# Kernel optimization log

Hardware: AMD Instinct MI355X
Metric: run time of the kernel (lower is better)

Reference implementation:

```python
import jax, jax.numpy as jnp
from jax import lax
import numpy as np

H = 512
W = 512
SIGMA = 0.1
IN_CH = [3, 66, 64, 64, 32, 32, 32, 16, 16]
OUT_CH = [64, 64, 64, 32, 32, 32, 16, 16, 16]
N_LAYERS = 9


def setup_inputs() -> dict:
    key = jax.random.key(0)
    ks = jax.random.split(key, 32)
    inp = {}
    inp['x'] = jax.random.uniform(ks[0], (3, 3, 1, 1), jnp.float32)  # query + 2 neighbor coords
    inp['neighbors'] = jax.random.uniform(ks[1], (2, 3, H, W), jnp.float32)
    inp['albedo_index'] = 4
    for i in range(N_LAYERS):
        kh = 1 if i == 0 else 3
        fan_in = IN_CH[i] * kh * kh
        inp[f'w{i}'] = jax.random.normal(ks[2 + i], (OUT_CH[i], IN_CH[i], kh, kh), jnp.float32) / np.sqrt(fan_in).astype(np.float32)
        inp[f'b{i}'] = jnp.zeros((OUT_CH[i],), jnp.float32)
    inp['wf'] = jax.random.normal(ks[20], (6, 16, 3, 3), jnp.float32) / np.sqrt(16 * 9).astype(np.float32)
    inp['bf'] = jnp.zeros((6,), jnp.float32)
    inp['albedos'] = 0.5 + jax.random.uniform(ks[21], (9, 3, H, W), jnp.float32)
    return inp


def _conv(x, w, b):
    y = lax.conv_general_dilated(x, w, (1, 1), 'VALID', dimension_numbers=('NCHW', 'OIHW', 'NCHW'))
    return y + b[None, :, None, None]


def _decoder(x, ws, bs, wf, bf):
    # coordconv constant [[ [0,2],[0,2] ], [ [0,0],[2,2] ]] with shape [2,2,2]
    coordconv = jnp.array([[[0., 2.], [0., 2.]], [[0., 0.], [2., 2.]]], dtype=x.dtype)
    for i in range(N_LAYERS):
        x = jnp.repeat(jnp.repeat(x, 2, axis=2), 2, axis=3)  # nearest upsample x2
        if i > 0:
            x = jnp.pad(x, ((0, 0), (0, 0), (1, 1), (1, 1)), mode='reflect')
        x = jax.nn.leaky_relu(_conv(x, ws[i], bs[i]), 0.01)
        if i == 0:
            cc = jnp.broadcast_to(coordconv[None], (x.shape[0],) + coordconv.shape)
            x = jnp.concatenate([x, cc], axis=1)  # -> 66 channels at 2x2
    x = jnp.pad(x, ((0, 0), (0, 0), (1, 1), (1, 1)), mode='reflect')
    return jnp.tanh(_conv(x, wf, bf))  # [B, 6, H, W]


def _grid_sample_border(img, grid):
    # bilinear, padding_mode='border', align_corners=False (matches torch grid_sample)
    N, C, Hh, Ww = img.shape
    gx = jnp.clip((grid[..., 0] + 1.0) * Ww / 2.0 - 0.5, 0.0, Ww - 1.0)
    gy = jnp.clip((grid[..., 1] + 1.0) * Hh / 2.0 - 0.5, 0.0, Hh - 1.0)
    x0 = jnp.floor(gx)
    y0 = jnp.floor(gy)
    wx = (gx - x0)[:, None]  # [N,1,H,W]
    wy = (gy - y0)[:, None]
    x0i = jnp.clip(x0.astype(jnp.int32), 0, Ww - 1)
    x1i = jnp.clip(x0i + 1, 0, Ww - 1)
    y0i = jnp.clip(y0.astype(jnp.int32), 0, Hh - 1)
    y1i = jnp.clip(y0i + 1, 0, Hh - 1)
    g = jax.vmap(lambda im, yi, xi: im[:, yi, xi])
    v00 = g(img, y0i, x0i)
    v01 = g(img, y0i, x1i)
    v10 = g(img, y1i, x0i)
    v11 = g(img, y1i, x1i)
    return v00 * (1 - wx) * (1 - wy) + v01 * wx * (1 - wy) + v10 * (1 - wx) * wy + v11 * wx * wy


def _blending(x, neighbors, flows, albedo):
    eps = 1e-5
    light_flow, view_flow, time_flow = flows[:1, 0:2], flows[:1, 2:4], flows[:1, 4:6]
    lf_n, vf_n, tf_n = flows[1:, 0:2], flows[1:, 2:4], flows[1:, 4:6]
    delta = x[:1] - x[1:]  # [2,3,1,1], broadcasts in place of torch.tile
    dl, dv, dt = delta[:, 0:1], delta[:, 1:2], delta[:, 2:3]
    flag = (jnp.abs(dl) > 0).astype(flows.dtype)
    offset_fwd = dl * light_flow + dv * view_flow + dt * time_flow  # [2,2,H,W]
    shading = flag * neighbors / albedo + (1 - flag) * neighbors
    ys = jnp.linspace(-1.0, 1.0, H)
    xs = jnp.linspace(-1.0, 1.0, W)
    grid_base = jnp.stack(jnp.meshgrid(xs, ys, indexing='xy'), axis=-1)  # [H,W,2], (...,0)=x
    grid = grid_base[None] + offset_fwd.transpose(0, 2, 3, 1)  # [2,H,W,2]
    warped_shading = _grid_sample_border(shading, grid)
    warped_vf = _grid_sample_border(vf_n, grid)
    warped_tf = _grid_sample_border(tf_n, grid)
    warped_lf = _grid_sample_border(lf_n, grid)
    warped_image = flag * warped_shading * albedo + (1 - flag) * warped_shading
    offset_bwd = dl * warped_lf + dv * warped_vf + dt * warped_tf
    dist = jnp.sum(jnp.abs(offset_fwd - offset_bwd), axis=1, keepdims=True)
    weight = jnp.exp(-SIGMA * W * dist)
    wn = weight / (jnp.sum(weight, axis=0, keepdims=True) + eps)
    return jnp.sum(warped_image * wn, axis=0, keepdims=True)  # [1,3,H,W]


def reference(x, neighbors, albedo_index, w0, w1, w2, w3, w4, w5, w6, w7, w8,
              b0, b1, b2, b3, b4, b5, b6, b7, b8, wf, bf, albedos):
    ws = [w0, w1, w2, w3, w4, w5, w6, w7, w8]
    bs = [b0, b1, b2, b3, b4, b5, b6, b7, b8]
    flows = _decoder(x, ws, bs, wf, bf)
    albedo = albedos[albedo_index]  # [3,H,W]
    return _blending(x, neighbors, flows, albedo)
```

## Files before the change

### kernel.cpp

```cpp
#include <hip/hip_runtime.h>
#include <hip/hip_bf16.h>
#include <math.h>


#define HH 512
#define WWI 512
#define HWP (HH*WWI)

__device__ __forceinline__ int xcd_swz(int bx, int nbx) {
  if ((nbx & 7) == 0) {
    int c = nbx >> 3;
    return (bx & 7) * c + (bx >> 3);
  }
  return bx;
}

__global__ void k_layer0(const float* __restrict__ xin, const float* __restrict__ w,
                         const float* __restrict__ bias, float* __restrict__ out)
{
  for (int idx = threadIdx.x; idx < 3*66*4; idx += blockDim.x) {
    int pos = idx & 3;
    int c = (idx >> 2) % 66;
    int b = idx / (66*4);
    float v;
    if (c < 64) {
      float a = bias[c];
      #pragma unroll
      for (int ci = 0; ci < 3; ci++) a += w[c*3+ci] * xin[b*3+ci];
      v = (a >= 0.f) ? a : 0.01f*a;
    } else {
      int xx = pos & 1, yy = pos >> 1;
      v = (c == 64) ? 2.f*(float)xx : 2.f*(float)yy;
    }
    out[idx] = v;
  }
}

__global__ void k_foldw8(const float* __restrict__ w1, const float* __restrict__ w2,
                         const float* __restrict__ w3, const float* __restrict__ w4,
                         const float* __restrict__ w5, const float* __restrict__ w6,
                         const float* __restrict__ w7, const float* __restrict__ w8,
                         float* __restrict__ f1, float* __restrict__ f2,
                         float* __restrict__ f3, float* __restrict__ f4,
                         float* __restrict__ f5, float* __restrict__ f6,
                         float* __restrict__ f7, float* __restrict__ f8)
{
  int idx = blockIdx.x*blockDim.x + threadIdx.x;
  const float* w; float* f; int n;
  if      (idx < 4224)  { w = w1; f = f1; n = idx; }
  else if (idx < 8320)  { w = w2; f = f2; n = idx - 4224; }
  else if (idx < 10368) { w = w3; f = f3; n = idx - 8320; }
  else if (idx < 11392) { w = w4; f = f4; n = idx - 10368; }
  else if (idx < 12416) { w = w5; f = f5; n = idx - 11392; }
  else if (idx < 12928) { w = w6; f = f6; n = idx - 12416; }
  else if (idx < 13184) { w = w7; f = f7; n = idx - 12928; }
  else if (idx < 13440) { w = w8; f = f8; n = idx - 13184; }
  else return;

  const float* ws = w + (size_t)n*9;
  float W[9];
  #pragma unroll
  for (int k = 0; k < 9; k++) W[k] = ws[k];

  float a[2][2][3];
  #pragma unroll
  for (int c = 0; c < 3; c++) {
    a[0][0][c] = W[c];          a[0][1][c] = W[3+c] + W[6+c];
    a[1][0][c] = W[c] + W[3+c]; a[1][1][c] = W[6+c];
  }
  float* fo = f + (size_t)n*16;
  #pragma unroll
  for (int py = 0; py < 2; py++)
    #pragma unroll
    for (int px = 0; px < 2; px++) {
      int p = py*2 + px;
      #pragma unroll
      for (int ky = 0; ky < 2; ky++) {
        float kx0 = (px == 0) ? a[py][ky][0] : (a[py][ky][0] + a[py][ky][1]);
        float kx1 = (px == 0) ? (a[py][ky][1] + a[py][ky][2]) : a[py][ky][2];
        fo[p*4 + ky*2 + 0] = kx0;
        fo[p*4 + ky*2 + 1] = kx1;
      }
    }
}

template<int CIN>
__global__ void k_upconv_s(const float* __restrict__ in, float* __restrict__ out,
                           const float* __restrict__ wfold, const float* __restrict__ bias,
                           int B, int CO, int Hin)
{
  extern __shared__ float4 wlds4[];
  int nt = blockDim.x, tid = threadIdx.x;
  int co = blockIdx.y;
  const int stride = CIN + 1;
  const float4* wsrc = reinterpret_cast<const float4*>(wfold);
  for (int s = tid; s < CIN*4; s += nt) {
    int p = s & 3;
    int ci = s >> 2;
    wlds4[p*stride + ci] = wsrc[(size_t)(co*CIN + ci)*4 + p];
  }
  __syncthreads();

  int Hout = Hin * 2;
  int npix = B * Hout * Hout;
  int idx = blockIdx.x*nt + tid;
  if (idx >= npix) return;
  int x = idx % Hout;
  int y = (idx / Hout) % Hout;
  int b = idx / (Hout * Hout);

  int X = x >> 1, Y = y >> 1;
  int px = x & 1, py = y & 1;

  int r_lo = py ? Y : (Y > 0 ? Y-1 : 0);
  int r_hi = py ? (Y < Hin-1 ? Y+1 : Hin-1) : Y;
  int c_lo = px ? X : (X > 0 ? X-1 : 0);
  int c_hi = px ? (X < Hin-1 ? X+1 : Hin-1) : X;

  float acc = bias[co];

  const size_t plane = (size_t)Hin * Hin;
  const float* ibase = in + (size_t)b * CIN * plane;
  const float4* wb = wlds4 + (py*2 + px) * stride;

  #pragma unroll 4
  for (int ci = 0; ci < CIN; ci++) {
    const float* ip = ibase + (size_t)ci * plane;
    const float* rl = ip + (size_t)r_lo * Hin;
    const float* rh = ip + (size_t)r_hi * Hin;
    float4 w4 = wb[ci];
    acc += w4.x*rl[c_lo] + w4.y*rl[c_hi] + w4.z*rh[c_lo] + w4.w*rh[c_hi];
  }

  float v = (acc >= 0.f) ? acc : 0.01f*acc;
  out[((size_t)b*CO + co)*((size_t)Hout*Hout) + (size_t)y*Hout + x] = v;
}

template<int COB, int P>
__global__ void k_upconv_wP(const float* __restrict__ in, float* __restrict__ out,
                            const float* __restrict__ wfold, const float* __restrict__ bias,
                            int B, int Cin, int CO, int Hin)
{
  extern __shared__ float4 wlds4[];
  int nt = blockDim.x, tid = threadIdx.x;
  int co0 = blockIdx.y * COB;
  int stride = Cin * COB + 1;
  int nw = Cin * COB * 4;
  const float4* wsrc = reinterpret_cast<const float4*>(wfold);
  for (int s = tid; s < nw; s += nt) {
    int p = s & 3;
    int r = s >> 2;
    int ci = r % Cin;
    int col = r / Cin;
    wlds4[p*stride + ci*COB + col] = wsrc[(size_t)((co0 + col)*Cin + ci)*4 + p];
  }
  __syncthreads();

  int Hout = Hin * 2;
  int q = Hout / P;
  int total = B * Hout * q;
  int bx = xcd_swz(blockIdx.x, gridDim.x);
  int idx = bx*nt + tid;
  if (idx >= total) return;
  int x1 = idx % q;
  int y  = (idx / q) % Hout;
  int b  = idx / (q * Hout);

  int px = x1 & 1, py = y & 1;
  int Y = y >> 1;
  int r_lo = py ? Y : (Y > 0 ? Y-1 : 0);
  int r_hi = py ? (Y < Hin-1 ? Y+1 : Hin-1) : Y;

  int clo[P], chi[P];
  #pragma unroll
  for (int k = 0; k < P; k++) {
    int X = (x1 + k*q) >> 1;
    clo[k] = px ? X : (X > 0 ? X-1 : 0);
    chi[k] = px ? (X < Hin-1 ? X+1 : Hin-1) : X;
  }

  float acc[P][COB];
  #pragma unroll
  for (int j = 0; j < COB; j++) {
    float bv = bias[co0 + j];
    #pragma unroll
    for (int k = 0; k < P; k++) acc[k][j] = bv;
  }

  const size_t plane = (size_t)Hin * Hin;
  const float* ibase = in + (size_t)b * Cin * plane;
  const float4* wb = wlds4 + (py*2 + px) * stride;

  for (int ci = 0; ci < Cin; ci++) {
    const float* ip = ibase + (size_t)ci * plane;
    const float* rl = ip + (size_t)r_lo * Hin;
    const float* rh = ip + (size_t)r_hi * Hin;
    float pl0[P], pl1[P], ph0[P], ph1[P];
    #pragma unroll
    for (int k = 0; k < P; k++) {
      pl0[k] = rl[clo[k]]; pl1[k] = rl[chi[k]];
      ph0[k] = rh[clo[k]]; ph1[k] = rh[chi[k]];
    }
    const float4* wc = wb + ci * COB;
    #pragma unroll
    for (int j = 0; j < COB; j++) {
      float4 w4 = wc[j];
      #pragma unroll
      for (int k = 0; k < P; k++)
        acc[k][j] += w4.x*pl0[k] + w4.y*pl1[k] + w4.z*ph0[k] + w4.w*ph1[k];
    }
  }

  size_t oplane = (size_t)Hout * Hout;
  float* op = out + ((size_t)b * CO + co0) * oplane + (size_t)y*Hout + x1;
  #pragma unroll
  for (int j = 0; j < COB; j++) {
    #pragma unroll
    for (int k = 0; k < P; k++) {
      float v = acc[k][j];
      v = (v >= 0.f) ? v : 0.01f*v;
      op[k*q] = v;
    }
    op += oplane;
  }
}

__global__ void k_final2(const float* __restrict__ in, float* __restrict__ out,
                         const float* __restrict__ w, const float* __restrict__ bias)
{
  int total = 3 * HH * (WWI/2);
  int bx = xcd_swz(blockIdx.x, gridDim.x);
  int idx = bx*blockDim.x + threadIdx.x;
  if (idx >= total) return;
  int xh = idx % (WWI/2);
  int y  = (idx / (WWI/2)) % HH;
  int b  = idx / (HH * (WWI/2));
  int x0 = 2*xh;

  int ry[3];
  #pragma unroll
  for (int d = 0; d < 3; d++) {
    int t = y - 1 + d;
    t = (t < 0) ? -t : t;
    ry[d] = (t >= HH) ? (2*(HH-1) - t) : t;
  }
  int cx[4];
  cx[0] = (x0 == 0) ? 1 : x0-1;
  cx[1] = x0;
  cx[2] = x0+1;
  cx[3] = (x0+2 >= WWI) ? (2*(WWI-1) - (x0+2)) : x0+2;

  float acc0[6], acc1[6];
  #pragma unroll
  for (int co = 0; co < 6; co++) { float bv = bias[co]; acc0[co] = bv; acc1[co] = bv; }

  for (int ci = 0; ci < 16; ci++) {
    const float* ib = in + ((size_t)(b*16) + ci) * HWP;
    float p[3][4];
    #pragma unroll
    for (int dy = 0; dy < 3; dy++) {
      const float* r = ib + (size_t)ry[dy]*WWI;
      #pragma unroll
      for (int dx = 0; dx < 4; dx++) p[dy][dx] = r[cx[dx]];
    }
    const float* wc = w + ci*9;
    #pragma unroll
    for (int co = 0; co < 6; co++) {
      const float* wcc = wc + co*16*9;
      #pragma unroll
      for (int dy = 0; dy < 3; dy++) {
        #pragma unroll
        for (int dx = 0; dx < 3; dx++) {
          float wv = wcc[dy*3+dx];
          acc0[co] += wv * p[dy][dx];
          acc1[co] += wv * p[dy][dx+1];
        }
      }
    }
  }

  size_t pix = (size_t)y*WWI + x0;
  #pragma unroll
  for (int co = 0; co < 6; co++) {
    float2 v = make_float2(tanhf(acc0[co]), tanhf(acc1[co]));
    *reinterpret_cast<float2*>(out + ((size_t)(b*6) + co)*HWP + pix) = v;
  }
}

__global__ void k_blend(const float* __restrict__ xin, const float* __restrict__ neighbors,
                        const int* __restrict__ aidx, const float* __restrict__ albedos,
                        const float* __restrict__ flows, float* __restrict__ out)
{
  int idx = blockIdx.x*blockDim.x + threadIdx.x;
  if (idx >= HWP) return;
  int xo = idx & (WWI-1);
  int yo = idx >> 9;

  float xv[9];
  #pragma unroll
  for (int i = 0; i < 9; i++) xv[i] = xin[i];

  float f0[6];
  #pragma unroll
  for (int c = 0; c < 6; c++) f0[c] = flows[(size_t)c*HWP + idx];

  const float* alb = albedos + (size_t)aidx[0]*3*HWP;
  float albp[3];
  #pragma unroll
  for (int ch = 0; ch < 3; ch++) albp[ch] = alb[(size_t)ch*HWP + idx];

  float num0 = 0.f, num1 = 0.f, num2 = 0.f;
  float wsum = 0.f;

  #pragma unroll
  for (int n = 0; n < 2; n++) {
    float dl = xv[0] - xv[(n+1)*3 + 0];
    float dv = xv[1] - xv[(n+1)*3 + 1];
    float dt = xv[2] - xv[(n+1)*3 + 2];
    bool fl = fabsf(dl) > 0.f;

    float ofx = dl*f0[0] + dv*f0[2] + dt*f0[4];
    float ofy = dl*f0[1] + dv*f0[3] + dt*f0[5];

    float gx = ((-1.f + (2.f/511.f)*(float)xo) + ofx + 1.f)*256.f - 0.5f;
    float gy = ((-1.f + (2.f/511.f)*(float)yo) + ofy + 1.f)*256.f - 0.5f;
    gx = fminf(fmaxf(gx, 0.f), 511.f);
    gy = fminf(fmaxf(gy, 0.f), 511.f);

    float x0f = floorf(gx), y0f = floorf(gy);
    float wx = gx - x0f, wy = gy - y0f;
    int x0i = (int)x0f, y0i = (int)y0f;
    int x1i = min(x0i + 1, WWI-1), y1i = min(y0i + 1, HH-1);

    float cw[4] = {(1.f-wx)*(1.f-wy), wx*(1.f-wy), (1.f-wx)*wy, wx*wy};
    int   cp[4] = {y0i*WWI + x0i, y0i*WWI + x1i, y1i*WWI + x0i, y1i*WWI + x1i};

    const float* nb = neighbors + (size_t)n*3*HWP;
    const float* Fn = flows + (size_t)(n+1)*6*HWP;

    float s0=0.f,s1=0.f,s2=0.f;
    float l0=0.f,l1=0.f,v0=0.f,v1=0.f,t0=0.f,t1=0.f;
    #pragma unroll
    for (int c = 0; c < 4; c++) {
      int p = cp[c];
      float ww = cw[c];
      float n0 = nb[p];
      float n1 = nb[HWP + p];
      float n2 = nb[2*HWP + p];
      if (fl) {
        n0 /= alb[p];
        n1 /= alb[HWP + p];
        n2 /= alb[2*HWP + p];
      }
      s0 += ww*n0; s1 += ww*n1; s2 += ww*n2;
      l0 += ww*Fn[p];             l1 += ww*Fn[HWP + p];
      v0 += ww*Fn[2*HWP + p];     v1 += ww*Fn[3*HWP + p];
      t0 += ww*Fn[4*HWP + p];     t1 += ww*Fn[5*HWP + p];
    }

    float wi0 = fl ? s0*albp[0] : s0;
    float wi1 = fl ? s1*albp[1] : s1;
    float wi2 = fl ? s2*albp[2] : s2;

    float obx = dl*l0 + dv*v0 + dt*t0;
    float oby = dl*l1 + dv*v1 + dt*t1;
    float dist = fabsf(ofx - obx) + fabsf(ofy - oby);
    float wgt = expf(-51.2f * dist);

    wsum += wgt;
    num0 += wgt*wi0; num1 += wgt*wi1; num2 += wgt*wi2;
  }

  float inv = 1.f / (wsum + 1e-5f);
  out[idx]         = num0*inv;
  out[HWP + idx]   = num1*inv;
  out[2*HWP + idx] = num2*inv;
}

extern "C" void kernel_launch(void* const* d_in, const int* in_sizes, int n_in,
                              void* d_out, int out_size, void* d_ws, size_t ws_size,
                              hipStream_t stream) {
  const float* x         = (const float*)d_in[0];
  const float* neighbors = (const float*)d_in[1];
  const int*   aidx      = (const int*)d_in[2];
  const float* wts[10];
  const float* bis[10];
  for (int i = 0; i < 9; i++) { wts[i] = (const float*)d_in[3+2*i]; bis[i] = (const float*)d_in[4+2*i]; }
  wts[9] = (const float*)d_in[21];
  bis[9] = (const float*)d_in[22];
  const float* albedos = (const float*)d_in[23];

  float* wk   = (float*)d_ws;
  float* bufS = wk;
  float* bufA = wk + 800;
  float* bufB = bufA + 4718592;
  size_t need = (size_t)(800 + 4718592 + 12582912) * 4;
  if (ws_size < need) return;

  float* wf1 = bufA + 3200000;
  float* wf2 = wf1 + 67584;
  float* wf3 = wf2 + 65536;
  float* wf4 = wf3 + 32768;
  float* wf5 = wf4 + 16384;
  float* wf6 = wf5 + 16384;
  float* wf7 = wf6 + 8192;
  float* wf8 = wf7 + 4096;
  k_foldw8<<<53, 256, 0, stream>>>(wts[1], wts[2], wts[3], wts[4], wts[5], wts[6], wts[7], wts[8],
                                   wf1, wf2, wf3, wf4, wf5, wf6, wf7, wf8);

  k_layer0<<<1, 256, 0, stream>>>(x, wts[0], bis[0], bufS);

  auto blocks = [](int total){ return (total + 255) / 256; };

  {
    dim3 g1(blocks(3*4*4), 64), g2(blocks(3*8*8), 64);
    dim3 g3(blocks(3*16*16), 32), g4(blocks(3*32*32), 32), g5(blocks(3*64*64), 32);
    k_upconv_s<66><<<g1, 256, (size_t)4*(66+1)*16, stream>>>(bufS, bufA, wf1, bis[1], 3, 64, 2);
    k_upconv_s<64><<<g2, 256, (size_t)4*(64+1)*16, stream>>>(bufA, bufB, wf2, bis[2], 3, 64, 4);
    k_upconv_s<64><<<g3, 256, (size_t)4*(64+1)*16, stream>>>(bufB, bufA, wf3, bis[3], 3, 32, 8);
    k_upconv_s<32><<<g4, 256, (size_t)4*(32+1)*16, stream>>>(bufA, bufB, wf4, bis[4], 3, 32, 16);
    k_upconv_s<32><<<g5, 256, (size_t)4*(32+1)*16, stream>>>(bufB, bufA, wf5, bis[5], 3, 32, 32);
  }

  {
    dim3 g6(blocks(3*128*32), 4);
    dim3 g7(blocks(3*256*64), 4);
    dim3 g8(blocks(3*512*128), 4);
    k_upconv_wP<4,4><<<g6, 256, (size_t)4*(32*4+1)*16, stream>>>(bufA, bufB, wf6, bis[6], 3, 32, 16, 64);
    k_upconv_wP<4,4><<<g7, 256, (size_t)4*(16*4+1)*16, stream>>>(bufB, bufA, wf7, bis[7], 3, 16, 16, 128);
    k_upconv_wP<4,4><<<g8, 256, (size_t)4*(16*4+1)*16, stream>>>(bufA, bufB, wf8, bis[8], 3, 16, 16, 256);
  }

  k_final2<<<blocks(3*HH*(WWI/2)), 256, 0, stream>>>(bufB, bufA, wts[9], bis[9]);
  k_blend<<<blocks(HWP), 256, 0, stream>>>(x, neighbors, aidx, albedos, bufA, (float*)d_out);
}
```

Before: 280.9 us.

## Merge prep kernels and fuse decoder layers 1-5 into one cooperative kernel

Merges weight folding and layer-0 into a single prep kernel. Replaces the five small upconv launches for layers 1-5 with one persistent cooperative kernel of 768 blocks that loops over (chunk, channel) work units and uses grid-wide syncs between layers. This is meant to remove per-launch overhead and idle gaps for tiny early layers. In exchange it adds grid.sync barriers, per-unit weight reloads into shared memory, and relies on cooperative launch co-residency.

```diff
diff --git a/kernel.cpp b/kernel.cpp
--- a/kernel.cpp
+++ b/kernel.cpp
@@ -1,6 +1,9 @@
 #include <hip/hip_runtime.h>
 #include <hip/hip_bf16.h>
+#include <hip/hip_cooperative_groups.h>
 #include <math.h>
+
+namespace cg = cooperative_groups;
 
 
 #define HH 512
@@ -15,48 +18,8 @@
   return bx;
 }
 
-__global__ void k_layer0(const float* __restrict__ xin, const float* __restrict__ w,
-                         const float* __restrict__ bias, float* __restrict__ out)
-{
-  for (int idx = threadIdx.x; idx < 3*66*4; idx += blockDim.x) {
-    int pos = idx & 3;
-    int c = (idx >> 2) % 66;
-    int b = idx / (66*4);
-    float v;
-    if (c < 64) {
-      float a = bias[c];
-      #pragma unroll
-      for (int ci = 0; ci < 3; ci++) a += w[c*3+ci] * xin[b*3+ci];
-      v = (a >= 0.f) ? a : 0.01f*a;
-    } else {
-      int xx = pos & 1, yy = pos >> 1;
-      v = (c == 64) ? 2.f*(float)xx : 2.f*(float)yy;
-    }
-    out[idx] = v;
-  }
-}
-
-__global__ void k_foldw8(const float* __restrict__ w1, const float* __restrict__ w2,
-                         const float* __restrict__ w3, const float* __restrict__ w4,
-                         const float* __restrict__ w5, const float* __restrict__ w6,
-                         const float* __restrict__ w7, const float* __restrict__ w8,
-                         float* __restrict__ f1, float* __restrict__ f2,
-                         float* __restrict__ f3, float* __restrict__ f4,
-                         float* __restrict__ f5, float* __restrict__ f6,
-                         float* __restrict__ f7, float* __restrict__ f8)
-{
-  int idx = blockIdx.x*blockDim.x + threadIdx.x;
-  const float* w; float* f; int n;
-  if      (idx < 4224)  { w = w1; f = f1; n = idx; }
-  else if (idx < 8320)  { w = w2; f = f2; n = idx - 4224; }
-  else if (idx < 10368) { w = w3; f = f3; n = idx - 8320; }
-  else if (idx < 11392) { w = w4; f = f4; n = idx - 10368; }
-  else if (idx < 12416) { w = w5; f = f5; n = idx - 11392; }
-  else if (idx < 12928) { w = w6; f = f6; n = idx - 12416; }
-  else if (idx < 13184) { w = w7; f = f7; n = idx - 12928; }
-  else if (idx < 13440) { w = w8; f = f8; n = idx - 13184; }
-  else return;
-
+__device__ __forceinline__ void fold_one(const float* __restrict__ w, float* __restrict__ f, int n)
+{
   const float* ws = w + (size_t)n*9;
   float W[9];
   #pragma unroll
@@ -84,56 +47,133 @@
     }
 }
 
+__global__ void k_prep(const float* __restrict__ x, const float* __restrict__ w0,
+                       const float* __restrict__ b0, float* __restrict__ outS,
+                       const float* __restrict__ w1, const float* __restrict__ w2,
+                       const float* __restrict__ w3, const float* __restrict__ w4,
+                       const float* __restrict__ w5, const float* __restrict__ w6,
+                       const float* __restrict__ w7, const float* __restrict__ w8,
+                       float* __restrict__ f1, float* __restrict__ f2,
+                       float* __restrict__ f3, float* __restrict__ f4,
+                       float* __restrict__ f5, float* __restrict__ f6,
+                       float* __restrict__ f7, float* __restrict__ f8)
+{
+  if (blockIdx.x < 53) {
+    int idx = blockIdx.x*blockDim.x + threadIdx.x;
+    const float* w; float* f; int n;
+    if      (idx < 4224)  { w = w1; f = f1; n = idx; }
+    else if (idx < 8320)  { w = w2; f = f2; n = idx - 4224; }
+    else if (idx < 10368) { w = w3; f = f3; n = idx - 8320; }
+    else if (idx < 11392) { w = w4; f = f4; n = idx - 10368; }
+    else if (idx < 12416) { w = w5; f = f5; n = idx - 11392; }
+    else if (idx < 12928) { w = w6; f = f6; n = idx - 12416; }
+    else if (idx < 13184) { w = w7; f = f7; n = idx - 12928; }
+    else if (idx < 13440) { w = w8; f = f8; n = idx - 13184; }
+    else return;
+    fold_one(w, f, n);
+  } else {
+    for (int idx = threadIdx.x; idx < 3*66*4; idx += blockDim.x) {
+      int pos = idx & 3;
+      int c = (idx >> 2) % 66;
+      int b = idx / (66*4);
+      float v;
+      if (c < 64) {
+        float a = b0[c];
+        #pragma unroll
+        for (int ci = 0; ci < 3; ci++) a += w0[c*3+ci] * x[b*3+ci];
+        v = (a >= 0.f) ? a : 0.01f*a;
+      } else {
+        int xx = pos & 1, yy = pos >> 1;
+        v = (c == 64) ? 2.f*(float)xx : 2.f*(float)yy;
+      }
+      outS[idx] = v;
+    }
+  }
+}
+
 template<int CIN>
-__global__ void k_upconv_s(const float* __restrict__ in, float* __restrict__ out,
-                           const float* __restrict__ wfold, const float* __restrict__ bias,
-                           int B, int CO, int Hin)
-{
-  extern __shared__ float4 wlds4[];
-  int nt = blockDim.x, tid = threadIdx.x;
-  int co = blockIdx.y;
+__device__ void phase_up(const float* __restrict__ in, float* __restrict__ out,
+                         const float* __restrict__ wfold, const float* __restrict__ bias,
+                         int CO, int Hin, float4* wlds, int nblocks)
+{
+  const int B = 3;
+  int Hout = Hin * 2;
+  int npix = B * Hout * Hout;
+  int chunks = (npix + 255) >> 8;
+  int units = chunks * CO;
+  int tid = threadIdx.x;
   const int stride = CIN + 1;
   const float4* wsrc = reinterpret_cast<const float4*>(wfold);
-  for (int s = tid; s < CIN*4; s += nt) {
-    int p = s & 3;
-    int ci = s >> 2;
-    wlds4[p*stride + ci] = wsrc[(size_t)(co*CIN + ci)*4 + p];
-  }
-  __syncthreads();
-
-  int Hout = Hin * 2;
-  int npix = B * Hout * Hout;
-  int idx = blockIdx.x*nt + tid;
-  if (idx >= npix) return;
-  int x = idx % Hout;
-  int y = (idx / Hout) % Hout;
-  int b = idx / (Hout * Hout);
-
-  int X = x >> 1, Y = y >> 1;
-  int px = x & 1, py = y & 1;
-
-  int r_lo = py ? Y : (Y > 0 ? Y-1 : 0);
-  int r_hi = py ? (Y < Hin-1 ? Y+1 : Hin-1) : Y;
-  int c_lo = px ? X : (X > 0 ? X-1 : 0);
-  int c_hi = px ? (X < Hin-1 ? X+1 : Hin-1) : X;
-
-  float acc = bias[co];
-
-  const size_t plane = (size_t)Hin * Hin;
-  const float* ibase = in + (size_t)b * CIN * plane;
-  const float4* wb = wlds4 + (py*2 + px) * stride;
-
-  #pragma unroll 4
-  for (int ci = 0; ci < CIN; ci++) {
-    const float* ip = ibase + (size_t)ci * plane;
-    const float* rl = ip + (size_t)r_lo * Hin;
-    const float* rh = ip + (size_t)r_hi * Hin;
-    float4 w4 = wb[ci];
-    acc += w4.x*rl[c_lo] + w4.y*rl[c_hi] + w4.z*rh[c_lo] + w4.w*rh[c_hi];
-  }
-
-  float v = (acc >= 0.f) ? acc : 0.01f*acc;
-  out[((size_t)b*CO + co)*((size_t)Hout*Hout) + (size_t)y*Hout + x] = v;
+
+  for (int u = blockIdx.x; u < units; u += nblocks) {
+    int co = u % CO;
+    int chunk = u / CO;
+
+    for (int s = tid; s < CIN*4; s += 256) {
+      int p = s & 3;
+      int ci = s >> 2;
+      wlds[p*stride + ci] = wsrc[(size_t)(co*CIN + ci)*4 + p];
+    }
+    __syncthreads();
+
+    int idx = chunk*256 + tid;
+    if (idx < npix) {
+      int x = idx % Hout;
+      int y = (idx / Hout) % Hout;
+      int b = idx / (Hout * Hout);
+
+      int X = x >> 1, Y = y >> 1;
+      int px = x & 1, py = y & 1;
+
+      int r_lo = py ? Y : (Y > 0 ? Y-1 : 0);
+      int r_hi = py ? (Y < Hin-1 ? Y+1 : Hin-1) : Y;
+      int c_lo = px ? X : (X > 0 ? X-1 : 0);
+      int c_hi = px ? (X < Hin-1 ? X+1 : Hin-1) : X;
+
+      float acc = bias[co];
+
+      const size_t plane = (size_t)Hin * Hin;
+      const float* ibase = in + (size_t)b * CIN * plane;
+      const float4* wb = wlds + (py*2 + px) * stride;
+
+      #pragma unroll 4
+      for (int ci = 0; ci < CIN; ci++) {
+        const float* ip = ibase + (size_t)ci * plane;
+        const float* rl = ip + (size_t)r_lo * Hin;
+        const float* rh = ip + (size_t)r_hi * Hin;
+        float4 w4 = wb[ci];
+        acc += w4.x*rl[c_lo] + w4.y*rl[c_hi] + w4.z*rh[c_lo] + w4.w*rh[c_hi];
+      }
+
+      float v = (acc >= 0.f) ? acc : 0.01f*acc;
+      out[((size_t)b*CO + co)*((size_t)Hout*Hout) + (size_t)y*Hout + x] = v;
+    }
+    __syncthreads();
+  }
+}
+
+__global__ __launch_bounds__(256)
+void k_L15(const float* __restrict__ bufS, float* __restrict__ bufA, float* __restrict__ bufB,
+           const float* __restrict__ wf1, const float* __restrict__ wf2,
+           const float* __restrict__ wf3, const float* __restrict__ wf4,
+           const float* __restrict__ wf5,
+           const float* __restrict__ b1, const float* __restrict__ b2,
+           const float* __restrict__ b3, const float* __restrict__ b4,
+           const float* __restrict__ b5)
+{
+  cg::grid_group grid = cg::this_grid();
+  __shared__ float4 swlds[268];
+  int nb = gridDim.x;
+
+  phase_up<66>(bufS, bufA, wf1, b1, 64, 2,  swlds, nb);
+  __threadfence(); grid.sync();
+  phase_up<64>(bufA, bufB, wf2, b2, 64, 4,  swlds, nb);
+  __threadfence(); grid.sync();
+  phase_up<64>(bufB, bufA, wf3, b3, 32, 8,  swlds, nb);
+  __threadfence(); grid.sync();
+  phase_up<32>(bufA, bufB, wf4, b4, 32, 16, swlds, nb);
+  __threadfence(); grid.sync();
+  phase_up<32>(bufB, bufA, wf5, b5, 32, 32, swlds, nb);
 }
 
 template<int COB, int P>
@@ -405,22 +445,26 @@
   float* wf6 = wf5 + 16384;
   float* wf7 = wf6 + 8192;
   float* wf8 = wf7 + 4096;
-  k_foldw8<<<53, 256, 0, stream>>>(wts[1], wts[2], wts[3], wts[4], wts[5], wts[6], wts[7], wts[8],
-                                   wf1, wf2, wf3, wf4, wf5, wf6, wf7, wf8);
-
-  k_layer0<<<1, 256, 0, stream>>>(x, wts[0], bis[0], bufS);
+
+  k_prep<<<54, 256, 0, stream>>>(x, wts[0], bis[0], bufS,
+                                 wts[1], wts[2], wts[3], wts[4], wts[5], wts[6], wts[7], wts[8],
+                                 wf1, wf2, wf3, wf4, wf5, wf6, wf7, wf8);
+
+  {
+    const float* a_bufS = bufS;
+    float* a_bufA = bufA;
+    float* a_bufB = bufB;
+    const float* a_wf1 = wf1; const float* a_wf2 = wf2; const float* a_wf3 = wf3;
+    const float* a_wf4 = wf4; const float* a_wf5 = wf5;
+    const float* a_b1 = bis[1]; const float* a_b2 = bis[2]; const float* a_b3 = bis[3];
+    const float* a_b4 = bis[4]; const float* a_b5 = bis[5];
+    void* cargs[] = { &a_bufS, &a_bufA, &a_bufB,
+                      &a_wf1, &a_wf2, &a_wf3, &a_wf4, &a_wf5,
+                      &a_b1, &a_b2, &a_b3, &a_b4, &a_b5 };
+    hipLaunchCooperativeKernel((void*)k_L15, dim3(768), dim3(256), cargs, 0, stream);
+  }
 
   auto blocks = [](int total){ return (total + 255) / 256; };
-
-  {
-    dim3 g1(blocks(3*4*4), 64), g2(blocks(3*8*8), 64);
-    dim3 g3(blocks(3*16*16), 32), g4(blocks(3*32*32), 32), g5(blocks(3*64*64), 32);
-    k_upconv_s<66><<<g1, 256, (size_t)4*(66+1)*16, stream>>>(bufS, bufA, wf1, bis[1], 3, 64, 2);
-    k_upconv_s<64><<<g2, 256, (size_t)4*(64+1)*16, stream>>>(bufA, bufB, wf2, bis[2], 3, 64, 4);
-    k_upconv_s<64><<<g3, 256, (size_t)4*(64+1)*16, stream>>>(bufB, bufA, wf3, bis[3], 3, 32, 8);
-    k_upconv_s<32><<<g4, 256, (size_t)4*(32+1)*16, stream>>>(bufA, bufB, wf4, bis[4], 3, 32, 16);
-    k_upconv_s<32><<<g5, 256, (size_t)4*(32+1)*16, stream>>>(bufB, bufA, wf5, bis[5], 3, 32, 32);
-  }
 
   {
     dim3 g6(blocks(3*128*32), 4);
```

Result: slower. 817.9 us (+191.2%).
